# Optimization experiments

Measured on AMD Instinct MI355X. Metric: run time of the kernel, lower is better.

Reference implementation:

```python
import jax, jax.numpy as jnp
import numpy as np

REFRACTORY_PERIOD = 5
DAMPENING_FACTOR = 0.3


def setup_inputs() -> dict:
    key = jax.random.key(0)
    B, T, N = 32, 4096, 256
    x = jax.random.normal(key, (B, T, N), dtype=jnp.float32)
    return {"x": x}


def _refractory_scan(x):
    # x: [B, T, N]; scan over time keeping refractory counter q resident.
    B, T, N = x.shape
    xt = jnp.swapaxes(x, 0, 1)  # [T, B, N]

    def step(q, x_t):
        cond = (x_t > 0) & (q == 0)
        z_t = jnp.where(cond, jnp.ones_like(q), jnp.zeros_like(q))
        q = jnp.maximum(jnp.zeros_like(q), q - 1) + REFRACTORY_PERIOD * z_t
        return q, z_t

    q0 = jnp.zeros((B, N), dtype=x.dtype)
    # Note: the t=0 case in the original (z0 = x0>0, q = R*z0) is exactly the
    # first step of this scan starting from q0 = 0.
    _, z = jax.lax.scan(step, q0, xt)
    return jnp.swapaxes(z, 0, 1)  # [B, T, N]


def reference(x) -> jnp.ndarray:
    # Forward value is exactly z_forward (the surrogate-gradient straight-through
    # construction leaves the value unchanged).
    return _refractory_scan(x)
```

## Files before the change

### kernel.cpp

```cpp
#include <hip/hip_runtime.h>
#include <cstdint>
#include <cstddef>

#define BB 32
#define TT 4096
#define NN 256
#define NNV 64
#define CC 32
#define PSUB 4
#define PP 128
#define PG 32

__global__ __launch_bounds__(256, 4) void refrac_scan(const float* __restrict__ x,
                                                      uint32_t* __restrict__ tbl,
                                                      uint32_t* __restrict__ bits_g) {
    const int tid = threadIdx.x;
    const int pg = blockIdx.x >> 5;
    const int b  = blockIdx.x & 31;
    const int psub = tid >> 6;
    const int n4 = tid & 63;
    const int p = pg * PSUB + psub;

    const float4* __restrict__ xv = reinterpret_cast<const float4*>(x)
        + ((size_t)b * TT + (size_t)p * CC) * NNV + n4;

    int na[4][6];
    #pragma unroll
    for (int c = 0; c < 4; ++c)
        #pragma unroll
        for (int e = 0; e < 6; ++e) na[c][e] = e;

    uint32_t cur[4] = {0u, 0u, 0u, 0u};

    #pragma unroll
    for (int jb = 0; jb < CC; jb += 8) {
        float4 buf[8];
        #pragma unroll
        for (int u = 0; u < 8; ++u)
            buf[u] = xv[(size_t)(jb + u) * NNV];
        #pragma unroll
        for (int u = 0; u < 8; ++u) {
            const int j = jb + u;
            const float4 v = buf[u];
            const float fv[4] = {v.x, v.y, v.z, v.w};
            #pragma unroll
            for (int c = 0; c < 4; ++c) {
                const bool pos = fv[c] > 0.0f;
                cur[c] |= pos ? (1u << j) : 0u;
                #pragma unroll
                for (int e = 0; e < 6; ++e)
                    if (pos & (j >= na[c][e])) na[c][e] = j + 6;
            }
        }
    }

    const size_t row = (size_t)b * PP + p;

    uint32_t t4[4];
    #pragma unroll
    for (int c = 0; c < 4; ++c) {
        uint32_t t = 0;
        #pragma unroll
        for (int e = 0; e < 6; ++e) {
            int q = na[c][e] - CC;
            q = q > 0 ? q : 0;
            t |= (uint32_t)q << (4 * e);
        }
        t4[c] = t;
    }
    reinterpret_cast<uint4*>(tbl)[row * NNV + n4] =
        make_uint4(t4[0], t4[1], t4[2], t4[3]);
    reinterpret_cast<uint4*>(bits_g)[row * NNV + n4] =
        make_uint4(cur[0], cur[1], cur[2], cur[3]);
}

__global__ __launch_bounds__(256) void refrac_compose(const uint32_t* __restrict__ tbl,
                                                      uint8_t* __restrict__ entry) {
    const int n = threadIdx.x;
    const int b = blockIdx.x;
    int e = 0;
    for (int pb = 0; pb < PP; pb += 16) {
        uint32_t tv[16];
        #pragma unroll
        for (int i = 0; i < 16; ++i)
            tv[i] = tbl[((size_t)b * PP + pb + i) * NN + n];
        #pragma unroll
        for (int i = 0; i < 16; ++i) {
            entry[((size_t)b * PP + pb + i) * NN + n] = (uint8_t)e;
            e = (int)((tv[i] >> (4 * e)) & 0xFu);
        }
    }
}

__global__ __launch_bounds__(256, 4) void refrac_emit(const uint32_t* __restrict__ bits_g,
                                                      const uint8_t* __restrict__ entry,
                                                      float* __restrict__ z) {
    const int tid = threadIdx.x;
    const int pg = blockIdx.x >> 5;
    const int b  = blockIdx.x & 31;
    const int psub = tid >> 6;
    const int n4 = tid & 63;
    const int p = pg * PSUB + psub;

    const size_t row = (size_t)b * PP + p;

    const uint32_t ew =
        reinterpret_cast<const uint32_t*>(entry)[row * NNV + n4];
    int ea[4];
    #pragma unroll
    for (int c = 0; c < 4; ++c) ea[c] = (int)((ew >> (8 * c)) & 0xFFu);

    const uint4 bv = reinterpret_cast<const uint4*>(bits_g)[row * NNV + n4];
    const uint32_t bw[4] = {bv.x, bv.y, bv.z, bv.w};

    float4* __restrict__ zv = reinterpret_cast<float4*>(z)
        + ((size_t)b * TT + (size_t)p * CC) * NNV + n4;

    #pragma unroll
    for (int j = 0; j < CC; ++j) {
        float o[4];
        #pragma unroll
        for (int c = 0; c < 4; ++c) {
            const bool sp = (((bw[c] >> j) & 1u) != 0u) & (j >= ea[c]);
            if (sp) ea[c] = j + 6;
            o[c] = sp ? 1.0f : 0.0f;
        }
        zv[(size_t)j * NNV] = make_float4(o[0], o[1], o[2], o[3]);
    }
}

extern "C" void kernel_launch(void* const* d_in, const int* in_sizes, int n_in,
                              void* d_out, int out_size, void* d_ws, size_t ws_size,
                              hipStream_t stream) {
    const float* x = (const float*)d_in[0];
    float* z = (float*)d_out;

    uint32_t* tbl = (uint32_t*)d_ws;
    uint32_t* bits_g = (uint32_t*)((char*)d_ws + (size_t)BB * PP * NN * 4);
    uint8_t*  entry  = (uint8_t*)((char*)d_ws + (size_t)BB * PP * NN * 8);

    refrac_scan<<<dim3(BB * PG), 256, 0, stream>>>(x, tbl, bits_g);
    refrac_compose<<<dim3(BB), 256, 0, stream>>>(tbl, entry);
    refrac_emit<<<dim3(BB * PG), 256, 0, stream>>>(bits_g, entry, z);
}
```

Measured before the change: 269.9 us.

## Replace per-chunk transfer tables with sequential bitmask trajectory via ctz

The first kernel now only packs sign bits into 32-bit masks, dropping the 6-entry state transfer table computation. A middle kernel walks each (b,n) sequence serially over 128 words, using count-trailing-zeros to find accepted spikes and carry the refractory offset. The final kernel just expands the spike bits to floats. This cuts ALU work in the parallel phases but makes the serial middle phase heavier, with up to 6 ctz iterations per word and only 8192 threads spread over 128 small blocks.

```diff
diff --git a/kernel.cpp b/kernel.cpp
--- a/kernel.cpp
+++ b/kernel.cpp
@@ -11,9 +11,8 @@
 #define PP 128
 #define PG 32
 
-__global__ __launch_bounds__(256, 4) void refrac_scan(const float* __restrict__ x,
-                                                      uint32_t* __restrict__ tbl,
-                                                      uint32_t* __restrict__ bits_g) {
+__global__ __launch_bounds__(256, 4) void sign_extract(const float* __restrict__ x,
+                                                       uint32_t* __restrict__ bits_g) {
     const int tid = threadIdx.x;
     const int pg = blockIdx.x >> 5;
     const int b  = blockIdx.x & 31;
@@ -24,77 +23,63 @@
     const float4* __restrict__ xv = reinterpret_cast<const float4*>(x)
         + ((size_t)b * TT + (size_t)p * CC) * NNV + n4;
 
-    int na[4][6];
-    #pragma unroll
-    for (int c = 0; c < 4; ++c)
-        #pragma unroll
-        for (int e = 0; e < 6; ++e) na[c][e] = e;
-
-    uint32_t cur[4] = {0u, 0u, 0u, 0u};
+    uint32_t cur0 = 0, cur1 = 0, cur2 = 0, cur3 = 0;
 
     #pragma unroll
-    for (int jb = 0; jb < CC; jb += 8) {
-        float4 buf[8];
+    for (int h = 0; h < 2; ++h) {
+        float4 buf[16];
         #pragma unroll
-        for (int u = 0; u < 8; ++u)
-            buf[u] = xv[(size_t)(jb + u) * NNV];
+        for (int u = 0; u < 16; ++u)
+            buf[u] = xv[(size_t)(h * 16 + u) * NNV];
         #pragma unroll
-        for (int u = 0; u < 8; ++u) {
-            const int j = jb + u;
-            const float4 v = buf[u];
-            const float fv[4] = {v.x, v.y, v.z, v.w};
-            #pragma unroll
-            for (int c = 0; c < 4; ++c) {
-                const bool pos = fv[c] > 0.0f;
-                cur[c] |= pos ? (1u << j) : 0u;
-                #pragma unroll
-                for (int e = 0; e < 6; ++e)
-                    if (pos & (j >= na[c][e])) na[c][e] = j + 6;
-            }
+        for (int u = 0; u < 16; ++u) {
+            const int j = h * 16 + u;
+            cur0 |= (buf[u].x > 0.0f) ? (1u << j) : 0u;
+            cur1 |= (buf[u].y > 0.0f) ? (1u << j) : 0u;
+            cur2 |= (buf[u].z > 0.0f) ? (1u << j) : 0u;
+            cur3 |= (buf[u].w > 0.0f) ? (1u << j) : 0u;
         }
     }
 
     const size_t row = (size_t)b * PP + p;
-
-    uint32_t t4[4];
-    #pragma unroll
-    for (int c = 0; c < 4; ++c) {
-        uint32_t t = 0;
-        #pragma unroll
-        for (int e = 0; e < 6; ++e) {
-            int q = na[c][e] - CC;
-            q = q > 0 ? q : 0;
-            t |= (uint32_t)q << (4 * e);
-        }
-        t4[c] = t;
-    }
-    reinterpret_cast<uint4*>(tbl)[row * NNV + n4] =
-        make_uint4(t4[0], t4[1], t4[2], t4[3]);
     reinterpret_cast<uint4*>(bits_g)[row * NNV + n4] =
-        make_uint4(cur[0], cur[1], cur[2], cur[3]);
+        make_uint4(cur0, cur1, cur2, cur3);
 }
 
-__global__ __launch_bounds__(256) void refrac_compose(const uint32_t* __restrict__ tbl,
-                                                      uint8_t* __restrict__ entry) {
-    const int n = threadIdx.x;
-    const int b = blockIdx.x;
-    int e = 0;
+__global__ __launch_bounds__(64) void trajectory(const uint32_t* __restrict__ bits_g,
+                                                 uint32_t* __restrict__ spk) {
+    const int g = blockIdx.x * 64 + threadIdx.x;
+    const int b = g >> 8;
+    const int n = g & 255;
+
+    int na = 0;
     for (int pb = 0; pb < PP; pb += 16) {
-        uint32_t tv[16];
+        uint32_t w[16];
         #pragma unroll
         for (int i = 0; i < 16; ++i)
-            tv[i] = tbl[((size_t)b * PP + pb + i) * NN + n];
+            w[i] = bits_g[((size_t)b * PP + pb + i) * NN + n];
         #pragma unroll
         for (int i = 0; i < 16; ++i) {
-            entry[((size_t)b * PP + pb + i) * NN + n] = (uint8_t)e;
-            e = (int)((tv[i] >> (4 * e)) & 0xFu);
+            uint32_t s = 0;
+            #pragma unroll
+            for (int it = 0; it < 6; ++it) {
+                const uint32_t m =
+                    (na < 32) ? (w[i] & (0xFFFFFFFFu << na)) : 0u;
+                if (m) {
+                    const int j = __builtin_ctz(m);
+                    s |= (1u << j);
+                    na = j + 6;
+                }
+            }
+            spk[((size_t)b * PP + pb + i) * NN + n] = s;
+            na -= 32;
+            if (na < 0) na = 0;
         }
     }
 }
 
-__global__ __launch_bounds__(256, 4) void refrac_emit(const uint32_t* __restrict__ bits_g,
-                                                      const uint8_t* __restrict__ entry,
-                                                      float* __restrict__ z) {
+__global__ __launch_bounds__(256, 4) void expand(const uint32_t* __restrict__ spk,
+                                                 float* __restrict__ z) {
     const int tid = threadIdx.x;
     const int pg = blockIdx.x >> 5;
     const int b  = blockIdx.x & 31;
@@ -103,29 +88,19 @@
     const int p = pg * PSUB + psub;
 
     const size_t row = (size_t)b * PP + p;
-
-    const uint32_t ew =
-        reinterpret_cast<const uint32_t*>(entry)[row * NNV + n4];
-    int ea[4];
-    #pragma unroll
-    for (int c = 0; c < 4; ++c) ea[c] = (int)((ew >> (8 * c)) & 0xFFu);
-
-    const uint4 bv = reinterpret_cast<const uint4*>(bits_g)[row * NNV + n4];
-    const uint32_t bw[4] = {bv.x, bv.y, bv.z, bv.w};
+    const uint4 sv = reinterpret_cast<const uint4*>(spk)[row * NNV + n4];
+    const uint32_t w0 = sv.x, w1 = sv.y, w2 = sv.z, w3 = sv.w;
 
     float4* __restrict__ zv = reinterpret_cast<float4*>(z)
         + ((size_t)b * TT + (size_t)p * CC) * NNV + n4;
 
     #pragma unroll
     for (int j = 0; j < CC; ++j) {
-        float o[4];
-        #pragma unroll
-        for (int c = 0; c < 4; ++c) {
-            const bool sp = (((bw[c] >> j) & 1u) != 0u) & (j >= ea[c]);
-            if (sp) ea[c] = j + 6;
-            o[c] = sp ? 1.0f : 0.0f;
-        }
-        zv[(size_t)j * NNV] = make_float4(o[0], o[1], o[2], o[3]);
+        zv[(size_t)j * NNV] = make_float4(
+            ((w0 >> j) & 1u) ? 1.0f : 0.0f,
+            ((w1 >> j) & 1u) ? 1.0f : 0.0f,
+            ((w2 >> j) & 1u) ? 1.0f : 0.0f,
+            ((w3 >> j) & 1u) ? 1.0f : 0.0f);
     }
 }
 
@@ -135,11 +110,10 @@
     const float* x = (const float*)d_in[0];
     float* z = (float*)d_out;
 
-    uint32_t* tbl = (uint32_t*)d_ws;
-    uint32_t* bits_g = (uint32_t*)((char*)d_ws + (size_t)BB * PP * NN * 4);
-    uint8_t*  entry  = (uint8_t*)((char*)d_ws + (size_t)BB * PP * NN * 8);
+    uint32_t* bits_g = (uint32_t*)d_ws;
+    uint32_t* spk = (uint32_t*)((char*)d_ws + (size_t)BB * PP * NN * 4);
 
-    refrac_scan<<<dim3(BB * PG), 256, 0, stream>>>(x, tbl, bits_g);
-    refrac_compose<<<dim3(BB), 256, 0, stream>>>(tbl, entry);
-    refrac_emit<<<dim3(BB * PG), 256, 0, stream>>>(bits_g, entry, z);
+    sign_extract<<<dim3(BB * PG), 256, 0, stream>>>(x, bits_g);
+    trajectory<<<dim3(BB * NN / 64), 64, 0, stream>>>(bits_g, spk);
+    expand<<<dim3(BB * PG), 256, 0, stream>>>(spk, z);
 }
```

New measurement: 277.3 us. 2.7% more time.
